# Kernel tuning notes

Hardware: AMD Instinct MI355X
Metric: run time of the kernel (lower is better)

The kernel has to match this reference:

```python
import jax, jax.numpy as jnp
import numpy as np

B, T, L, H, NH, F, V, K = 8, 128, 12, 768, 12, 3072, 30522, 5
DH = H // NH
START, STOP = 3, 4  # tag_to_idx['<START>'], tag_to_idx['<STOP>']


def _ln(x, s, b):
    m = jnp.mean(x, -1, keepdims=True)
    v = jnp.var(x, -1, keepdims=True)
    return (x - m) * jax.lax.rsqrt(v + 1e-12) * s + b


def setup_inputs() -> dict:
    key = jax.random.key(0)
    ks = jax.random.split(key, 16)
    sc = 0.02
    rn = lambda k, shp: jax.random.normal(k, shp, jnp.float32) * sc
    inp = {
        'sentence': jax.random.randint(ks[0], (B, T), 0, V),
        'sentence_mask': jnp.ones((B, T), jnp.int32),
        'word_emb': rn(ks[1], (V, H)),
        'pos_emb': rn(ks[2], (T, H)),
        'type_emb': rn(ks[3], (2, H)),
        'emb_ln_s': jnp.ones((H,), jnp.float32),
        'emb_ln_b': jnp.zeros((H,), jnp.float32),
        'Wqkv': rn(ks[4], (L, H, 3 * H)), 'bqkv': jnp.zeros((L, 3 * H), jnp.float32),
        'Wo': rn(ks[5], (L, H, H)), 'bo': jnp.zeros((L, H), jnp.float32),
        'ln1_s': jnp.ones((L, H), jnp.float32), 'ln1_b': jnp.zeros((L, H), jnp.float32),
        'W1': rn(ks[6], (L, H, F)), 'b1': jnp.zeros((L, F), jnp.float32),
        'W2': rn(ks[7], (L, F, H)), 'b2': jnp.zeros((L, H), jnp.float32),
        'ln2_s': jnp.ones((L, H), jnp.float32), 'ln2_b': jnp.zeros((L, H), jnp.float32),
        'Wt': rn(ks[8], (H, K)), 'bt': jnp.zeros((K,), jnp.float32),
    }
    trans = jax.random.normal(ks[9], (K, K), jnp.float32)
    # transitions[START, :] = -10000 ; transitions[:, STOP] = -10000
    trans = trans.at[START, :].set(-10000.0).at[:, STOP].set(-10000.0)
    inp['transitions'] = trans
    return inp


def _bert_feats(sentence, sentence_mask, word_emb, pos_emb, type_emb,
                emb_ln_s, emb_ln_b, Wqkv, bqkv, Wo, bo, ln1_s, ln1_b,
                W1, b1, W2, b2, ln2_s, ln2_b, Wt, bt):
    # embeddings (token_type_ids=None -> all zeros)
    x = word_emb[sentence] + pos_emb[None, :, :] + type_emb[0][None, None, :]
    x = _ln(x, emb_ln_s, emb_ln_b)
    # additive attention bias from padding mask
    bias = (1.0 - sentence_mask.astype(jnp.float32))[:, None, None, :] * -10000.0
    inv_sqrt_dh = 1.0 / np.sqrt(DH)

    def layer(h, p):
        wqkv, bqk, wo, bo_, s1, sb1, w1, wb1, w2, wb2, s2, sb2 = p
        qkv = h @ wqkv + bqk
        q, k, v = jnp.split(qkv, 3, axis=-1)
        q = q.reshape(B, T, NH, DH)
        k = k.reshape(B, T, NH, DH)
        v = v.reshape(B, T, NH, DH)
        att = jnp.einsum('bqhd,bkhd->bhqk', q, k) * inv_sqrt_dh + bias
        att = jax.nn.softmax(att, axis=-1)
        ctx = jnp.einsum('bhqk,bkhd->bqhd', att, v).reshape(B, T, H)
        h = _ln(h + ctx @ wo + bo_, s1, sb1)
        ff = jax.nn.gelu(h @ w1 + wb1) @ w2 + wb2
        h = _ln(h + ff, s2, sb2)
        return h, None

    x, _ = jax.lax.scan(layer, x, (Wqkv, bqkv, Wo, bo, ln1_s, ln1_b,
                                   W1, b1, W2, b2, ln2_s, ln2_b))
    # dropout(p=0.2) is identity at inference
    return x @ Wt + bt  # [B, T, K]


def _viterbi(feats, transitions):
    # feats: [B, T, K]; transitions[to, from]
    init = jnp.full((B, K), -10000.0, feats.dtype).at[:, START].set(0.0)

    def fwd_step(ld, feat_t):
        m = transitions[None, :, :] + ld[:, None, :]  # [B, K(to), K(from)]
        best = jnp.max(m, axis=-1)
        psi_t = jnp.argmax(m, axis=-1)
        return best + feat_t, psi_t

    feats_t = jnp.swapaxes(feats, 0, 1)  # [T, B, K]
    ld, psis = jax.lax.scan(fwd_step, init, feats_t[1:])  # psis: [T-1, B, K]
    score = jnp.max(ld, axis=-1)          # [B]
    last = jnp.argmax(ld, axis=-1)        # [B]

    def bwd_step(p, psi_t):
        prev = jnp.take_along_axis(psi_t, p[:, None], axis=-1)[:, 0]
        return prev, prev

    _, rest = jax.lax.scan(bwd_step, last, psis, reverse=True)  # [T-1, B]
    path = jnp.concatenate([rest, last[None, :]], axis=0).T     # [B, T]
    return score, path


def reference(sentence, sentence_mask, word_emb, pos_emb, type_emb,
              emb_ln_s, emb_ln_b, Wqkv, bqkv, Wo, bo, ln1_s, ln1_b,
              W1, b1, W2, b2, ln2_s, ln2_b, Wt, bt, transitions):
    feats = _bert_feats(sentence, sentence_mask, word_emb, pos_emb, type_emb,
                        emb_ln_s, emb_ln_b, Wqkv, bqkv, Wo, bo, ln1_s, ln1_b,
                        W1, b1, W2, b2, ln2_s, ln2_b, Wt, bt)
    score, path = _viterbi(feats, transitions)
    return score, path
```

## Files before the change

kernel.cpp:

```cpp
#include <hip/hip_runtime.h>
#include <cstdint>
#include <cstddef>

#define BB 8
#define TT 128
#define LL 12
#define HH 768
#define NHH 12
#define DHH 64
#define FFI 3072
#define KT 5
#define START_TAG 3
#define MTOK (BB*TT)

#define LQS 1769472u
#define LOS 589824u
#define L1S 2359296u
#define L2S 2359296u

typedef _Float16 f16x8 __attribute__((ext_vector_type(8)));
typedef _Float16 f16x4 __attribute__((ext_vector_type(4)));
typedef float f32x4 __attribute__((ext_vector_type(4)));

__device__ __forceinline__ void gl_lds16(const _Float16* g, _Float16* l) {
    __builtin_amdgcn_global_load_lds(
        (const __attribute__((address_space(1))) unsigned int*)g,
        (__attribute__((address_space(3))) unsigned int*)l, 16, 0, 0);
}

__device__ __forceinline__ float gelu_f(float x) {
    float c = 0.7978845608028654f * (x + 0.044715f * x * x * x);
    return 0.5f * x * (1.f + tanhf(c));
}

__device__ __forceinline__ void write_h_planes(const float* rowbuf, int tok,
                                               _Float16* dh, _Float16* dl, int c) {
    int kb = c >> 2;
    int rowm = tok & 127, mb = tok >> 7;
    int koct = c & 3;
    int p = rowm * 4 + (koct ^ (rowm & 3));
    size_t tb = ((size_t)(mb * 24 + kb)) * 4096;
    f16x8 vh, vl;
#pragma unroll
    for (int j = 0; j < 8; ++j) {
        float x = rowbuf[c * 8 + j];
        _Float16 hi = (_Float16)x;
        vh[j] = hi;
        vl[j] = (_Float16)((x - (float)hi) * 4096.f);
    }
    *(f16x8*)(dh + tb + (size_t)p * 8) = vh;
    *(f16x8*)(dl + tb + (size_t)p * 8) = vl;
}

__global__ __launch_bounds__(256) void embed_ln_kernel(
    const int* __restrict__ sentence,
    const float* __restrict__ word_emb,
    const float* __restrict__ pos_emb,
    const float* __restrict__ type_emb,
    const float* __restrict__ ln_s,
    const float* __restrict__ ln_b,
    float* __restrict__ h,
    _Float16* __restrict__ dh, _Float16* __restrict__ dl)
{
    int tok = blockIdx.x;
    int t = tok % TT;
    int id = sentence[tok];
    const float* we = word_emb + (size_t)id * HH;
    const float* pe = pos_emb + (size_t)t * HH;

    __shared__ float rowbuf[HH];
    __shared__ float rs_[4], rss_[4];
    float x[3];
    float s = 0.f, ss = 0.f;
#pragma unroll
    for (int i = 0; i < 3; ++i) {
        int d = threadIdx.x + i * 256;
        float v = we[d] + pe[d] + type_emb[d];
        x[i] = v; s += v; ss += v * v;
    }
    for (int o = 32; o; o >>= 1) { s += __shfl_down(s, o); ss += __shfl_down(ss, o); }
    int wid = threadIdx.x >> 6;
    if ((threadIdx.x & 63) == 0) { rs_[wid] = s; rss_[wid] = ss; }
    __syncthreads();
    s = rs_[0] + rs_[1] + rs_[2] + rs_[3];
    ss = rss_[0] + rss_[1] + rss_[2] + rss_[3];
    float mean = s * (1.f / HH);
    float var = ss * (1.f / HH) - mean * mean;
    float rstd = rsqrtf(var + 1e-12f);
#pragma unroll
    for (int i = 0; i < 3; ++i) {
        int d = threadIdx.x + i * 256;
        float y = (x[i] - mean) * rstd * ln_s[d] + ln_b[d];
        h[(size_t)tok * HH + d] = y;
        rowbuf[d] = y;
    }
    __syncthreads();
    if (threadIdx.x < 96) write_h_planes(rowbuf, tok, dh, dl, threadIdx.x);
}

template<int FEATS>
__global__ __launch_bounds__(256) void add_ln_red_kernel(
    float* __restrict__ h, const float* __restrict__ parts,
    const float* __restrict__ bias,
    const float* __restrict__ ln_s, const float* __restrict__ ln_b,
    _Float16* __restrict__ dh, _Float16* __restrict__ dl,
    const float* __restrict__ Wt, const float* __restrict__ bt,
    float* __restrict__ feats)
{
    int tok = blockIdx.x;
    __shared__ float rowbuf[HH];
    __shared__ float rs_[4], rss_[4];
    float x[3];
    float s = 0.f, ss = 0.f;
#pragma unroll
    for (int i = 0; i < 3; ++i) {
        int d = threadIdx.x + i * 256;
        size_t idx = (size_t)tok * HH + d;
        float delta = parts[idx] + parts[idx + (size_t)MTOK * HH]
                    + parts[idx + 2 * (size_t)MTOK * HH] + parts[idx + 3 * (size_t)MTOK * HH]
                    + bias[d];
        float v = h[idx] + delta;
        x[i] = v; s += v; ss += v * v;
    }
    for (int o = 32; o; o >>= 1) { s += __shfl_down(s, o); ss += __shfl_down(ss, o); }
    int wid = threadIdx.x >> 6;
    if ((threadIdx.x & 63) == 0) { rs_[wid] = s; rss_[wid] = ss; }
    __syncthreads();
    s = rs_[0] + rs_[1] + rs_[2] + rs_[3];
    ss = rss_[0] + rss_[1] + rss_[2] + rss_[3];
    float mean = s * (1.f / HH);
    float var = ss * (1.f / HH) - mean * mean;
    float rstd = rsqrtf(var + 1e-12f);
    float yv[3];
#pragma unroll
    for (int i = 0; i < 3; ++i) {
        int d = threadIdx.x + i * 256;
        float y = (x[i] - mean) * rstd * ln_s[d] + ln_b[d];
        yv[i] = y;
        if constexpr (!FEATS) {
            h[(size_t)tok * HH + d] = y;
            rowbuf[d] = y;
        }
    }
    if constexpr (!FEATS) {
        __syncthreads();
        if (threadIdx.x < 96) write_h_planes(rowbuf, tok, dh, dl, threadIdx.x);
    } else {
        float pt[5] = {0.f, 0.f, 0.f, 0.f, 0.f};
#pragma unroll
        for (int i = 0; i < 3; ++i) {
            int d = threadIdx.x + i * 256;
#pragma unroll
            for (int t = 0; t < 5; ++t) pt[t] += yv[i] * Wt[d * 5 + t];
        }
#pragma unroll
        for (int t = 0; t < 5; ++t)
            for (int o = 32; o; o >>= 1) pt[t] += __shfl_down(pt[t], o);
        __shared__ float fred[4][5];
        if ((threadIdx.x & 63) == 0)
#pragma unroll
            for (int t = 0; t < 5; ++t) fred[wid][t] = pt[t];
        __syncthreads();
        if (threadIdx.x < 5) {
            float fs = fred[0][threadIdx.x] + fred[1][threadIdx.x]
                     + fred[2][threadIdx.x] + fred[3][threadIdx.x] + bt[threadIdx.x];
            feats[tok * 5 + threadIdx.x] = fs;
        }
    }
}

template<int ALL>
__global__ __launch_bounds__(256) void wconv_kernel(
    const float* __restrict__ Wqkv, const float* __restrict__ Wo,
    const float* __restrict__ W1, const float* __restrict__ W2,
    _Float16* __restrict__ qh, _Float16* __restrict__ ql,
    _Float16* __restrict__ oh, _Float16* __restrict__ ol,
    _Float16* __restrict__ f1h, _Float16* __restrict__ f1l,
    _Float16* __restrict__ f2h, _Float16* __restrict__ f2l)
{
    int bb = blockIdx.x;
    int l = ALL ? bb / 3456 : 0;
    int b = ALL ? bb % 3456 : bb;
    const float* src; _Float16 *dh, *dl; int N, kTi, idx;
    if (b < 864)       { idx = b;        src = Wqkv + (size_t)l * 768 * 2304; dh = qh  + (size_t)l * LQS; dl = ql  + (size_t)l * LQS; N = 2304; kTi = 24; }
    else if (b < 1152) { idx = b - 864;  src = Wo   + (size_t)l * 768 * 768;  dh = oh  + (size_t)l * LOS; dl = ol  + (size_t)l * LOS; N = 768;  kTi = 24; }
    else if (b < 2304) { idx = b - 1152; src = W1   + (size_t)l * 768 * 3072; dh = f1h + (size_t)l * L1S; dl = f1l + (size_t)l * L1S; N = 3072; kTi = 24; }
    else               { idx = b - 2304; src = W2   + (size_t)l * 3072 * 768; dh = f2h + (size_t)l * L2S; dl = f2l + (size_t)l * L2S; N = 768;  kTi = 96; }
    int nb = idx / kTi, kb = idx % kTi;

    __shared__ float tile[32][65];
    const float* s0 = src + (size_t)(kb * 32) * N + nb * 64;
#pragma unroll
    for (int i = 0; i < 8; ++i) {
        int q = threadIdx.x + i * 256;
        int kk = q >> 6, n = q & 63;
        tile[kk][n] = s0[(size_t)kk * N + n];
    }
    __syncthreads();
    int p = threadIdx.x;
    int n = p >> 2, koct = (p & 3) ^ (n & 3);
    f16x8 vh, vl;
#pragma unroll
    for (int j = 0; j < 8; ++j) {
        float x = tile[koct * 8 + j][n];
        _Float16 hi = (_Float16)x;
        vh[j] = hi;
        vl[j] = (_Float16)((x - (float)hi) * 4096.f);
    }
    size_t tb = (size_t)idx * 2048;
    *(f16x8*)(dh + tb + (size_t)p * 8) = vh;
    *(f16x8*)(dl + tb + (size_t)p * 8) = vl;
}

template<int MODE>
__global__ __launch_bounds__(256) void mfma_gemm(
    const _Float16* __restrict__ Ah, const _Float16* __restrict__ Al,
    const _Float16* __restrict__ Bh, const _Float16* __restrict__ Bl,
    const float* __restrict__ bias, float* __restrict__ outF,
    _Float16* __restrict__ o1h, _Float16* __restrict__ o1l,
    _Float16* __restrict__ o2h, _Float16* __restrict__ o2l,
    int N, int kTi, int kpz)
{
    constexpr bool TRANS = (MODE >= 2);
    __shared__ _Float16 lds[2][12288];
    int tid = threadIdx.x, lane = tid & 63, w = tid >> 6;
    int wm = w >> 1, wn = w & 1;
    int mb = blockIdx.y, nb = blockIdx.x;
    int ktBeg = TRANS ? 0 : blockIdx.z * kpz;
    int ktEnd = TRANS ? kTi : ktBeg + kpz;

    const _Float16 *aTh, *aTl, *bTh, *bTl;
    if constexpr (!TRANS) {
        aTh = Ah + (size_t)mb * kTi * 4096;
        aTl = Al + (size_t)mb * kTi * 4096;
        bTh = Bh + (size_t)nb * kTi * 2048;
        bTl = Bl + (size_t)nb * kTi * 2048;
    } else {
        aTh = Ah + (size_t)(2 * mb) * kTi * 2048;
        aTl = Al + (size_t)(2 * mb) * kTi * 2048;
        bTh = Bh + (size_t)(nb >> 1) * kTi * 4096 + (nb & 1) * 2048;
        bTl = Bl + (size_t)(nb >> 1) * kTi * 4096 + (nb & 1) * 2048;
    }

    f32x4 acch[4][2], accc[4][2];
#pragma unroll
    for (int i = 0; i < 4; ++i)
#pragma unroll
        for (int j = 0; j < 2; ++j) { acch[i][j] = (f32x4)0.f; accc[i][j] = (f32x4)0.f; }

    auto stage = [&](int buf, int kt) {
#pragma unroll
        for (int j = 0; j < 6; ++j) {
            int i = w * 6 + j;
            const _Float16* src;
            if constexpr (!TRANS) {
                if (i < 8)       src = aTh + (size_t)kt * 4096 + i * 512;
                else if (i < 16) src = aTl + (size_t)kt * 4096 + (i - 8) * 512;
                else if (i < 20) src = bTh + (size_t)kt * 2048 + (i - 16) * 512;
                else             src = bTl + (size_t)kt * 2048 + (i - 20) * 512;
            } else {
                if (i < 8)       src = aTh + (size_t)(i >> 2) * kTi * 2048 + (size_t)kt * 2048 + (i & 3) * 512;
                else if (i < 16) src = aTl + (size_t)((i - 8) >> 2) * kTi * 2048 + (size_t)kt * 2048 + ((i - 8) & 3) * 512;
                else if (i < 20) src = bTh + (size_t)kt * 4096 + (i - 16) * 512;
                else             src = bTl + (size_t)kt * 4096 + (i - 20) * 512;
            }
            gl_lds16(src + lane * 8, &lds[buf][i * 512]);
        }
    };

    stage(0, ktBeg);
    stage(1, ktBeg + 1);
    int lm = lane & 15, lk = lane >> 4;
    for (int kt = ktBeg; kt < ktEnd; ++kt) {
        int cur = (kt - ktBeg) & 1;
        if (kt + 1 < ktEnd) { asm volatile("s_waitcnt vmcnt(6)" ::: "memory"); }
        else                { asm volatile("s_waitcnt vmcnt(0)" ::: "memory"); }
        __builtin_amdgcn_s_barrier();
        __builtin_amdgcn_sched_barrier(0);
        const char* lb = (const char*)&lds[cur][0];
        f16x8 ahf[4], alf[4], bhf[2], blf[2];
#pragma unroll
        for (int mi = 0; mi < 4; ++mi) {
            int row = wm * 64 + mi * 16 + lm;
            int off = (row * 64 + lk * 16) ^ ((row & 3) << 4);
            ahf[mi] = *(const f16x8*)(lb + off);
            alf[mi] = *(const f16x8*)(lb + 8192 + off);
        }
#pragma unroll
        for (int ni = 0; ni < 2; ++ni) {
            int nr = wn * 32 + ni * 16 + lm;
            int off = (nr * 64 + lk * 16) ^ ((nr & 3) << 4);
            bhf[ni] = *(const f16x8*)(lb + 16384 + off);
            blf[ni] = *(const f16x8*)(lb + 20480 + off);
        }
#pragma unroll
        for (int mi = 0; mi < 4; ++mi)
#pragma unroll
            for (int ni = 0; ni < 2; ++ni) {
                acch[mi][ni] = __builtin_amdgcn_mfma_f32_16x16x32_f16(ahf[mi], bhf[ni], acch[mi][ni], 0, 0, 0);
                accc[mi][ni] = __builtin_amdgcn_mfma_f32_16x16x32_f16(ahf[mi], blf[ni], accc[mi][ni], 0, 0, 0);
                accc[mi][ni] = __builtin_amdgcn_mfma_f32_16x16x32_f16(alf[mi], bhf[ni], accc[mi][ni], 0, 0, 0);
            }
        __builtin_amdgcn_sched_barrier(0);
        __builtin_amdgcn_s_barrier();
        if (kt + 2 < ktEnd) stage(cur, kt + 2);
    }

    const float inv = 1.0f / 4096.0f;
    if constexpr (MODE == 0) {
        float* Cz = outF + (size_t)blockIdx.z * 1024 * N;
#pragma unroll
        for (int mi = 0; mi < 4; ++mi)
#pragma unroll
            for (int ni = 0; ni < 2; ++ni) {
                int col = nb * 64 + wn * 32 + ni * 16 + lm;
                int r0 = mb * 128 + wm * 64 + mi * 16 + lk * 4;
#pragma unroll
                for (int j = 0; j < 4; ++j)
                    Cz[(size_t)(r0 + j) * N + col] = acch[mi][ni][j] + accc[mi][ni][j] * inv;
            }
    } else if constexpr (MODE == 2) {
        int region = mb / 6;
#pragma unroll
        for (int mi = 0; mi < 4; ++mi)
#pragma unroll
            for (int ni = 0; ni < 2; ++ni) {
                int n = mb * 128 + wm * 64 + mi * 16 + lk * 4;
                int tok = nb * 64 + wn * 32 + ni * 16 + lm;
                float4 bv = *(const float4*)(bias + n);
                float v[4];
#pragma unroll
                for (int j = 0; j < 4; ++j)
                    v[j] = acch[mi][ni][j] + accc[mi][ni][j] * inv + (&bv.x)[j];
                int b = tok >> 7, q = tok & 127;
                if (region < 2) {
                    int hh2 = (n >> 6) % 12, d = n & 63;
                    size_t img = (size_t)(b * 12 + hh2);
                    _Float16* dsth = (region == 0) ? o1h : o2h;
                    _Float16* dstl = (region == 0) ? o1l : o2l;
                    int byteo = q * 128 + ((d * 2) ^ ((q & 7) << 4));
                    f16x4 hi, lo;
#pragma unroll
                    for (int j = 0; j < 4; ++j) {
                        _Float16 hv = (_Float16)v[j];
                        hi[j] = hv; lo[j] = (_Float16)((v[j] - (float)hv) * 4096.f);
                    }
                    *(f16x4*)((char*)dsth + img * 16384 + byteo) = hi;
                    *(f16x4*)((char*)dstl + img * 16384 + byteo) = lo;
                } else {
                    int hh2 = (n - 1536) >> 6, d = n & 63;
                    float* vdst = outF + (size_t)(b * 12 + hh2) * 8192;
#pragma unroll
                    for (int j = 0; j < 4; ++j)
                        vdst[(size_t)(d + j) * 128 + q] = v[j];
                }
            }
    } else {
#pragma unroll
        for (int mi = 0; mi < 4; ++mi)
#pragma unroll
            for (int ni = 0; ni < 2; ++ni) {
                int n = mb * 128 + wm * 64 + mi * 16 + lk * 4;
                int tok = nb * 64 + wn * 32 + ni * 16 + lm;
                float4 bv = *(const float4*)(bias + n);
                int mbt = tok >> 7, rowm = tok & 127;
                int kb = n >> 5, koct = (n >> 3) & 3, half = (n >> 2) & 1;
                size_t eo = ((size_t)(mbt * 96 + kb)) * 4096
                          + (size_t)(rowm * 4 + (koct ^ (rowm & 3))) * 8 + half * 4;
                f16x4 hi, lo;
#pragma unroll
                for (int j = 0; j < 4; ++j) {
                    float x = gelu_f(acch[mi][ni][j] + accc[mi][ni][j] * inv + (&bv.x)[j]);
                    _Float16 hv = (_Float16)x;
                    hi[j] = hv; lo[j] = (_Float16)((x - (float)hv) * 4096.f);
                }
                *(f16x4*)(o1h + eo) = hi;
                *(f16x4*)(o1l + eo) = lo;
            }
    }
}

__global__ __launch_bounds__(256, 1) void attn_mfma(
    const _Float16* __restrict__ Qp_h, const _Float16* __restrict__ Qp_l,
    const _Float16* __restrict__ Kp_h, const _Float16* __restrict__ Kp_l,
    const float* __restrict__ vT, const int* __restrict__ mask,
    _Float16* __restrict__ cA_h, _Float16* __restrict__ cA_l)
{
    __shared__ __align__(16) char sm[82432];
    char* Kh  = sm;             char* Klo = sm + 16384;
    char* Qh  = sm + 32768;     char* Qlo = sm + 40960;
    char* Ph  = sm;             char* Plo = sm + 16384;
    char* Vth = sm + 49152;     char* Vtl = sm + 65536;
    float* biasf = (float*)(sm + 81920);

    int bx = blockIdx.x;
    int bh = bx >> 1, qh2 = bx & 1;
    int b = bh / 12, h = bh % 12;
    int q0 = qh2 * 64;
    int tid = threadIdx.x, lane = tid & 63, wv = tid >> 6;
    int lm = lane & 15, g = lane >> 4;
    int qr = wv * 16 + lm;
    const float inv = 1.0f / 4096.0f;

    {
        const _Float16* Ksh = Kp_h + (size_t)bh * 8192;
        const _Float16* Ksl = Kp_l + (size_t)bh * 8192;
        const _Float16* Qsh = Qp_h + (size_t)bh * 8192 + (size_t)q0 * 64;
        const _Float16* Qsl = Qp_l + (size_t)bh * 8192 + (size_t)q0 * 64;
#pragma unroll
        for (int i = 0; i < 4; ++i) {
            gl_lds16(Ksh + (size_t)(i * 256 + tid) * 8, (_Float16*)(Kh  + (i * 256 + tid) * 16));
            gl_lds16(Ksl + (size_t)(i * 256 + tid) * 8, (_Float16*)(Klo + (i * 256 + tid) * 16));
        }
#pragma unroll
        for (int i = 0; i < 2; ++i) {
            gl_lds16(Qsh + (size_t)(i * 256 + tid) * 8, (_Float16*)(Qh  + (i * 256 + tid) * 16));
            gl_lds16(Qsl + (size_t)(i * 256 + tid) * 8, (_Float16*)(Qlo + (i * 256 + tid) * 16));
        }
    }
    if (tid < 128) biasf[tid] = (1.f - (float)mask[b * 128 + tid]) * -10000.f;
    __syncthreads();

    f32x4 ah[8], ac[8];
#pragma unroll
    for (int i = 0; i < 8; ++i) { ah[i] = (f32x4)0.f; ac[i] = (f32x4)0.f; }
    __builtin_amdgcn_s_setprio(1);
#pragma unroll
    for (int ks = 0; ks < 2; ++ks) {
        int qoff = qr * 128 + ((ks * 64 + g * 16) ^ ((qr & 7) << 4));
        f16x8 q_h = *(const f16x8*)(Qh + qoff);
        f16x8 q_l = *(const f16x8*)(Qlo + qoff);
#pragma unroll
        for (int mf = 0; mf < 8; ++mf) {
            int kt = mf * 16 + lm;
            int koff = kt * 128 + ((ks * 64 + g * 16) ^ ((kt & 7) << 4));
            f16x8 k_h = *(const f16x8*)(Kh + koff);
            f16x8 k_l = *(const f16x8*)(Klo + koff);
            ah[mf] = __builtin_amdgcn_mfma_f32_16x16x32_f16(k_h, q_h, ah[mf], 0, 0, 0);
            ac[mf] = __builtin_amdgcn_mfma_f32_16x16x32_f16(k_h, q_l, ac[mf], 0, 0, 0);
            ac[mf] = __builtin_amdgcn_mfma_f32_16x16x32_f16(k_l, q_h, ac[mf], 0, 0, 0);
        }
    }
    __builtin_amdgcn_s_setprio(0);

    float kb_[8][4];
#pragma unroll
    for (int mf = 0; mf < 8; ++mf)
#pragma unroll
        for (int jj = 0; jj < 4; ++jj) kb_[mf][jj] = biasf[mf * 16 + g * 4 + jj];

    float pv_[8][4];
    float mx = -1e30f;
#pragma unroll
    for (int mf = 0; mf < 8; ++mf)
#pragma unroll
        for (int jj = 0; jj < 4; ++jj) {
            float s = (ah[mf][jj] + ac[mf][jj] * inv) * 0.125f + kb_[mf][jj];
            pv_[mf][jj] = s;
            mx = fmaxf(mx, s);
        }
    mx = fmaxf(mx, __shfl_xor(mx, 16));
    mx = fmaxf(mx, __shfl_xor(mx, 32));
    float sum = 0.f;
#pragma unroll
    for (int mf = 0; mf < 8; ++mf)
#pragma unroll
        for (int jj = 0; jj < 4; ++jj) {
            float e = expf(pv_[mf][jj] - mx);
            pv_[mf][jj] = e;
            sum += e;
        }
    sum += __shfl_xor(sum, 16);
    sum += __shfl_xor(sum, 32);
    float rs = 1.f / sum;
    __syncthreads();

#pragma unroll
    for (int mf = 0; mf < 8; ++mf) {
        f16x4 hi, lo;
#pragma unroll
        for (int jj = 0; jj < 4; ++jj) {
            float p = pv_[mf][jj] * rs;
            _Float16 hv = (_Float16)p;
            hi[jj] = hv; lo[jj] = (_Float16)((p - (float)hv) * 4096.f);
        }
        int byteo = qr * 256 + ((mf * 32 + g * 8) ^ ((qr & 7) << 4));
        *(f16x4*)(Ph + byteo) = hi;
        *(f16x4*)(Plo + byteo) = lo;
    }
    {
        int d = tid >> 2, tb = (tid & 3) * 32;
        const float* vsrc = vT + (size_t)bh * 8192 + (size_t)d * 128 + tb;
#pragma unroll
        for (int i = 0; i < 8; ++i) {
            float4 v = *(const float4*)(vsrc + i * 4);
            f16x4 hi, lo;
#pragma unroll
            for (int jj = 0; jj < 4; ++jj) {
                float x = (&v.x)[jj];
                _Float16 hv = (_Float16)x;
                hi[jj] = hv; lo[jj] = (_Float16)((x - (float)hv) * 4096.f);
            }
            int byteo = d * 256 + (((tb + i * 4) * 2) ^ ((d & 7) << 4));
            *(f16x4*)(Vth + byteo) = hi;
            *(f16x4*)(Vtl + byteo) = lo;
        }
    }
    __syncthreads();

    f32x4 ch[4], cc[4];
#pragma unroll
    for (int i = 0; i < 4; ++i) { ch[i] = (f32x4)0.f; cc[i] = (f32x4)0.f; }
    __builtin_amdgcn_s_setprio(1);
#pragma unroll
    for (int ks = 0; ks < 4; ++ks) {
        int poff = qr * 256 + ((ks * 64 + g * 16) ^ ((qr & 7) << 4));
        f16x8 p_h = *(const f16x8*)(Ph + poff);
        f16x8 p_l = *(const f16x8*)(Plo + poff);
#pragma unroll
        for (int mf = 0; mf < 4; ++mf) {
            int d = mf * 16 + lm;
            int voff = d * 256 + ((ks * 64 + g * 16) ^ ((d & 7) << 4));
            f16x8 vh = *(const f16x8*)(Vth + voff);
            f16x8 vl = *(const f16x8*)(Vtl + voff);
            ch[mf] = __builtin_amdgcn_mfma_f32_16x16x32_f16(vh, p_h, ch[mf], 0, 0, 0);
            cc[mf] = __builtin_amdgcn_mfma_f32_16x16x32_f16(vh, p_l, cc[mf], 0, 0, 0);
            cc[mf] = __builtin_amdgcn_mfma_f32_16x16x32_f16(vl, p_h, cc[mf], 0, 0, 0);
        }
    }
    __builtin_amdgcn_s_setprio(0);

    int q = q0 + qr;
#pragma unroll
    for (int mf = 0; mf < 4; ++mf) {
        int d0 = mf * 16 + g * 4;
        f16x4 hi, lo;
#pragma unroll
        for (int jj = 0; jj < 4; ++jj) {
            float x = ch[mf][jj] + cc[mf][jj] * inv;
            _Float16 hv = (_Float16)x;
            hi[jj] = hv; lo[jj] = (_Float16)((x - (float)hv) * 4096.f);
        }
        int kb = h * 2 + (d0 >> 5), koct = (d0 >> 3) & 3, half = (d0 >> 2) & 1;
        size_t eo = ((size_t)(b * 24 + kb)) * 4096
                  + (size_t)(q * 4 + (koct ^ (q & 3))) * 8 + half * 4;
        *(f16x4*)(cA_h + eo) = hi;
        *(f16x4*)(cA_l + eo) = lo;
    }
}

__global__ __launch_bounds__(64) void viterbi_kernel(
    const float* __restrict__ feats, const float* __restrict__ trans,
    float* __restrict__ out)
{
    __shared__ float tr[KT][KT];
    __shared__ unsigned char psi[TT - 1][BB][KT];
    int tid = threadIdx.x;
    if (tid < KT * KT) tr[tid / KT][tid % KT] = trans[tid];
    __syncthreads();
    if (tid < BB) {
        int b = tid;
        float ld[KT];
#pragma unroll
        for (int k = 0; k < KT; ++k) ld[k] = (k == START_TAG) ? 0.f : -10000.f;
        for (int t = 1; t < TT; ++t) {
            float nld[KT];
#pragma unroll
            for (int to = 0; to < KT; ++to) {
                float best = tr[to][0] + ld[0];
                int arg = 0;
#pragma unroll
                for (int fr = 1; fr < KT; ++fr) {
                    float v = tr[to][fr] + ld[fr];
                    if (v > best) { best = v; arg = fr; }
                }
                psi[t - 1][b][to] = (unsigned char)arg;
                nld[to] = best + feats[(size_t)(b * TT + t) * KT + to];
            }
#pragma unroll
            for (int k = 0; k < KT; ++k) ld[k] = nld[k];
        }
        float sc = ld[0]; int last = 0;
#pragma unroll
        for (int k = 1; k < KT; ++k) if (ld[k] > sc) { sc = ld[k]; last = k; }
        out[b] = sc;
        int p = last;
        out[BB + b * TT + (TT - 1)] = (float)last;
        for (int t = TT - 2; t >= 0; --t) {
            p = psi[t][b][p];
            out[BB + b * TT + t] = (float)p;
        }
    }
}

extern "C" void kernel_launch(void* const* d_in, const int* in_sizes, int n_in,
                              void* d_out, int out_size, void* d_ws, size_t ws_size,
                              hipStream_t stream) {
    const int*   sentence = (const int*)d_in[0];
    const int*   mask     = (const int*)d_in[1];
    const float* word_emb = (const float*)d_in[2];
    const float* pos_emb  = (const float*)d_in[3];
    const float* type_emb = (const float*)d_in[4];
    const float* emb_ln_s = (const float*)d_in[5];
    const float* emb_ln_b = (const float*)d_in[6];
    const float* Wqkv     = (const float*)d_in[7];
    const float* bqkv     = (const float*)d_in[8];
    const float* Wo       = (const float*)d_in[9];
    const float* bo       = (const float*)d_in[10];
    const float* ln1_s    = (const float*)d_in[11];
    const float* ln1_b    = (const float*)d_in[12];
    const float* W1       = (const float*)d_in[13];
    const float* b1       = (const float*)d_in[14];
    const float* W2       = (const float*)d_in[15];
    const float* b2       = (const float*)d_in[16];
    const float* ln2_s    = (const float*)d_in[17];
    const float* ln2_b    = (const float*)d_in[18];
    const float* Wt       = (const float*)d_in[19];
    const float* bt       = (const float*)d_in[20];
    const float* trans    = (const float*)d_in[21];

    char* base = (char*)d_ws;
    size_t off = 0;
    auto alloc = [&](size_t bytes) { void* p = base + off; off += (bytes + 255) & ~(size_t)255; return p; };

    const size_t planeElems = (size_t)(LQS + LOS + L1S + L2S);
    bool allL = ws_size >= (planeElems * 12 * 2 * 2 + (size_t)120 * 1024 * 1024);
    int NLL = allL ? 12 : 1;

    _Float16* wq_h = (_Float16*)alloc((size_t)LQS * NLL * 2);
    _Float16* wq_l = (_Float16*)alloc((size_t)LQS * NLL * 2);
    _Float16* wo_h = (_Float16*)alloc((size_t)LOS * NLL * 2);
    _Float16* wo_l = (_Float16*)alloc((size_t)LOS * NLL * 2);
    _Float16* w1_h = (_Float16*)alloc((size_t)L1S * NLL * 2);
    _Float16* w1_l = (_Float16*)alloc((size_t)L1S * NLL * 2);
    _Float16* w2_h = (_Float16*)alloc((size_t)L2S * NLL * 2);
    _Float16* w2_l = (_Float16*)alloc((size_t)L2S * NLL * 2);
    float* h       = (float*)alloc((size_t)MTOK * HH * 4);
    _Float16* hA_h = (_Float16*)alloc((size_t)MTOK * HH * 2);
    _Float16* hA_l = (_Float16*)alloc((size_t)MTOK * HH * 2);
    _Float16* Qp_h = (_Float16*)alloc((size_t)96 * 8192 * 2);
    _Float16* Qp_l = (_Float16*)alloc((size_t)96 * 8192 * 2);
    _Float16* Kp_h = (_Float16*)alloc((size_t)96 * 8192 * 2);
    _Float16* Kp_l = (_Float16*)alloc((size_t)96 * 8192 * 2);
    float* vT      = (float*)alloc((size_t)96 * 8192 * 4);
    _Float16* cA_h = (_Float16*)alloc((size_t)MTOK * HH * 2);
    _Float16* cA_l = (_Float16*)alloc((size_t)MTOK * HH * 2);
    _Float16* gA_h = (_Float16*)alloc((size_t)MTOK * FFI * 2);
    _Float16* gA_l = (_Float16*)alloc((size_t)MTOK * FFI * 2);
    float* parts   = (float*)alloc((size_t)4 * MTOK * HH * 4);
    float* featsb  = (float*)alloc((size_t)MTOK * KT * 4);

    embed_ln_kernel<<<MTOK, 256, 0, stream>>>(sentence, word_emb, pos_emb, type_emb,
                                              emb_ln_s, emb_ln_b, h, hA_h, hA_l);
    if (allL) {
        wconv_kernel<1><<<41472, 256, 0, stream>>>(
            Wqkv, Wo, W1, W2,
            wq_h, wq_l, wo_h, wo_l, w1_h, w1_l, w2_h, w2_l);
    }
    for (int l = 0; l < LL; ++l) {
        size_t qO = allL ? (size_t)l * LQS : 0;
        size_t oO = allL ? (size_t)l * LOS : 0;
        size_t f1O = allL ? (size_t)l * L1S : 0;
        size_t f2O = allL ? (size_t)l * L2S : 0;
        if (!allL) {
            wconv_kernel<0><<<3456, 256, 0, stream>>>(
                Wqkv + (size_t)l * 768 * 2304, Wo + (size_t)l * 768 * 768,
                W1 + (size_t)l * 768 * 3072, W2 + (size_t)l * 3072 * 768,
                wq_h, wq_l, wo_h, wo_l, w1_h, w1_l, w2_h, w2_l);
        }
        mfma_gemm<2><<<dim3(16, 18), 256, 0, stream>>>(
            wq_h + qO, wq_l + qO, hA_h, hA_l, bqkv + (size_t)l * 2304, vT,
            Qp_h, Qp_l, Kp_h, Kp_l, 0, 24, 24);
        attn_mfma<<<192, 256, 0, stream>>>(Qp_h, Qp_l, Kp_h, Kp_l, vT, mask, cA_h, cA_l);
        mfma_gemm<0><<<dim3(12, 8, 4), 256, 0, stream>>>(
            cA_h, cA_l, wo_h + oO, wo_l + oO, nullptr, parts,
            nullptr, nullptr, nullptr, nullptr, 768, 24, 6);
        add_ln_red_kernel<0><<<MTOK, 256, 0, stream>>>(
            h, parts, bo + (size_t)l * HH, ln1_s + (size_t)l * HH, ln1_b + (size_t)l * HH,
            hA_h, hA_l, nullptr, nullptr, nullptr);
        mfma_gemm<3><<<dim3(16, 24), 256, 0, stream>>>(
            w1_h + f1O, w1_l + f1O, hA_h, hA_l, b1 + (size_t)l * FFI, nullptr,
            gA_h, gA_l, nullptr, nullptr, 0, 24, 24);
        mfma_gemm<0><<<dim3(12, 8, 4), 256, 0, stream>>>(
            gA_h, gA_l, w2_h + f2O, w2_l + f2O, nullptr, parts,
            nullptr, nullptr, nullptr, nullptr, 768, 96, 24);
        if (l < LL - 1) {
            add_ln_red_kernel<0><<<MTOK, 256, 0, stream>>>(
                h, parts, b2 + (size_t)l * HH, ln2_s + (size_t)l * HH, ln2_b + (size_t)l * HH,
                hA_h, hA_l, nullptr, nullptr, nullptr);
        } else {
            add_ln_red_kernel<1><<<MTOK, 256, 0, stream>>>(
                h, parts, b2 + (size_t)l * HH, ln2_s + (size_t)l * HH, ln2_b + (size_t)l * HH,
                hA_h, hA_l, Wt, bt, featsb);
        }
    }
    viterbi_kernel<<<1, 64, 0, stream>>>(featsb, trans, (float*)d_out);
}
```

Before: 1.543 ms.

## Simplify GEMM double buffering, compute attention mask bias in registers, relax workspace check

The GEMM main loop changes from a two-stage prefetch, which used explicit vmcnt waits and raw barriers, to a simpler scheme. It stages the next tile at the top of each iteration and ends every iteration with a full __syncthreads. The attention kernel now reads the mask straight into registers instead of going through LDS, trims its shared memory, and raises the launch-bounds occupancy hint to 2. The all-layer weight conversion threshold becomes a fixed 384 MB check, and the N argument of two GEMM launches changes from 0 to 2304/3072. The simpler pipeline gives up prefetch depth, and with vmcnt waits removed the code relies on __syncthreads to cover the outstanding async LDS loads, which may also affect correctness.

New measurement: 1.630 ms. 1.06x slower.

```diff
diff --git a/kernel.cpp b/kernel.cpp
--- a/kernel.cpp
+++ b/kernel.cpp
@@ -269,15 +269,12 @@
     };
 
     stage(0, ktBeg);
-    stage(1, ktBeg + 1);
+    __syncthreads();
+    int buf = 0;
     int lm = lane & 15, lk = lane >> 4;
     for (int kt = ktBeg; kt < ktEnd; ++kt) {
-        int cur = (kt - ktBeg) & 1;
-        if (kt + 1 < ktEnd) { asm volatile("s_waitcnt vmcnt(6)" ::: "memory"); }
-        else                { asm volatile("s_waitcnt vmcnt(0)" ::: "memory"); }
-        __builtin_amdgcn_s_barrier();
-        __builtin_amdgcn_sched_barrier(0);
-        const char* lb = (const char*)&lds[cur][0];
+        if (kt + 1 < ktEnd) stage(buf ^ 1, kt + 1);
+        const char* lb = (const char*)&lds[buf][0];
         f16x8 ahf[4], alf[4], bhf[2], blf[2];
 #pragma unroll
         for (int mi = 0; mi < 4; ++mi) {
@@ -301,9 +298,8 @@
                 accc[mi][ni] = __builtin_amdgcn_mfma_f32_16x16x32_f16(ahf[mi], blf[ni], accc[mi][ni], 0, 0, 0);
                 accc[mi][ni] = __builtin_amdgcn_mfma_f32_16x16x32_f16(alf[mi], bhf[ni], accc[mi][ni], 0, 0, 0);
             }
-        __builtin_amdgcn_sched_barrier(0);
-        __builtin_amdgcn_s_barrier();
-        if (kt + 2 < ktEnd) stage(cur, kt + 2);
+        __syncthreads();
+        buf ^= 1;
     }
 
     const float inv = 1.0f / 4096.0f;
@@ -380,18 +376,17 @@
     }
 }
 
-__global__ __launch_bounds__(256, 1) void attn_mfma(
+__global__ __launch_bounds__(256, 2) void attn_mfma(
     const _Float16* __restrict__ Qp_h, const _Float16* __restrict__ Qp_l,
     const _Float16* __restrict__ Kp_h, const _Float16* __restrict__ Kp_l,
     const float* __restrict__ vT, const int* __restrict__ mask,
     _Float16* __restrict__ cA_h, _Float16* __restrict__ cA_l)
 {
-    __shared__ __align__(16) char sm[82432];
+    __shared__ __align__(16) char sm[81920];
     char* Kh  = sm;             char* Klo = sm + 16384;
     char* Qh  = sm + 32768;     char* Qlo = sm + 40960;
     char* Ph  = sm;             char* Plo = sm + 16384;
     char* Vth = sm + 49152;     char* Vtl = sm + 65536;
-    float* biasf = (float*)(sm + 81920);
 
     int bx = blockIdx.x;
     int bh = bx >> 1, qh2 = bx & 1;
@@ -418,7 +413,18 @@
             gl_lds16(Qsl + (size_t)(i * 256 + tid) * 8, (_Float16*)(Qlo + (i * 256 + tid) * 16));
         }
     }
-    if (tid < 128) biasf[tid] = (1.f - (float)mask[b * 128 + tid]) * -10000.f;
+    float kb_[8][4];
+    {
+        const int* mrow = mask + b * 128;
+#pragma unroll
+        for (int mf = 0; mf < 8; ++mf) {
+            int4 mv = *(const int4*)(mrow + mf * 16 + g * 4);
+            kb_[mf][0] = (1.f - (float)mv.x) * -10000.f;
+            kb_[mf][1] = (1.f - (float)mv.y) * -10000.f;
+            kb_[mf][2] = (1.f - (float)mv.z) * -10000.f;
+            kb_[mf][3] = (1.f - (float)mv.w) * -10000.f;
+        }
+    }
     __syncthreads();
 
     f32x4 ah[8], ac[8];
@@ -442,12 +448,6 @@
         }
     }
     __builtin_amdgcn_s_setprio(0);
-
-    float kb_[8][4];
-#pragma unroll
-    for (int mf = 0; mf < 8; ++mf)
-#pragma unroll
-        for (int jj = 0; jj < 4; ++jj) kb_[mf][jj] = biasf[mf * 16 + g * 4 + jj];
 
     float pv_[8][4];
     float mx = -1e30f;
@@ -623,8 +623,7 @@
     size_t off = 0;
     auto alloc = [&](size_t bytes) { void* p = base + off; off += (bytes + 255) & ~(size_t)255; return p; };
 
-    const size_t planeElems = (size_t)(LQS + LOS + L1S + L2S);
-    bool allL = ws_size >= (planeElems * 12 * 2 * 2 + (size_t)120 * 1024 * 1024);
+    bool allL = ws_size >= (384ULL << 20);
     int NLL = allL ? 12 : 1;
 
     _Float16* wq_h = (_Float16*)alloc((size_t)LQS * NLL * 2);
@@ -654,12 +653,11 @@
                                               emb_ln_s, emb_ln_b, h, hA_h, hA_l);
     if (allL) {
         wconv_kernel<1><<<41472, 256, 0, stream>>>(
-            Wqkv, Wo, W1, W2,
-            wq_h, wq_l, wo_h, wo_l, w1_h, w1_l, w2_h, w2_l);
+            Wqkv, Wo, W1, W2, wq_h, wq_l, wo_h, wo_l, w1_h, w1_l, w2_h, w2_l);
     }
     for (int l = 0; l < LL; ++l) {
-        size_t qO = allL ? (size_t)l * LQS : 0;
-        size_t oO = allL ? (size_t)l * LOS : 0;
+        size_t qO  = allL ? (size_t)l * LQS : 0;
+        size_t oO  = allL ? (size_t)l * LOS : 0;
         size_t f1O = allL ? (size_t)l * L1S : 0;
         size_t f2O = allL ? (size_t)l * L2S : 0;
         if (!allL) {
@@ -670,7 +668,7 @@
         }
         mfma_gemm<2><<<dim3(16, 18), 256, 0, stream>>>(
             wq_h + qO, wq_l + qO, hA_h, hA_l, bqkv + (size_t)l * 2304, vT,
-            Qp_h, Qp_l, Kp_h, Kp_l, 0, 24, 24);
+            Qp_h, Qp_l, Kp_h, Kp_l, 2304, 24, 24);
         attn_mfma<<<192, 256, 0, stream>>>(Qp_h, Qp_l, Kp_h, Kp_l, vT, mask, cA_h, cA_l);
         mfma_gemm<0><<<dim3(12, 8, 4), 256, 0, stream>>>(
             cA_h, cA_l, wo_h + oO, wo_l + oO, nullptr, parts,
@@ -680,7 +678,7 @@
             hA_h, hA_l, nullptr, nullptr, nullptr);
         mfma_gemm<3><<<dim3(16, 24), 256, 0, stream>>>(
             w1_h + f1O, w1_l + f1O, hA_h, hA_l, b1 + (size_t)l * FFI, nullptr,
-            gA_h, gA_l, nullptr, nullptr, 0, 24, 24);
+            gA_h, gA_l, nullptr, nullptr, 3072, 24, 24);
         mfma_gemm<0><<<dim3(12, 8, 4), 256, 0, stream>>>(
             gA_h, gA_l, w2_h + f2O, w2_l + f2O, nullptr, parts,
             nullptr, nullptr, nullptr, nullptr, 768, 96, 24);
```
